# Kernel optimization log

Measured on AMD Instinct MI355X. Metric: run time of the kernel, lower is better.

Reference implementation:

```python
import jax, jax.numpy as jnp
import numpy as np

HIDDEN = 4096
NUM_HEADS = 32
HEAD_DIM = HIDDEN // NUM_HEADS
B, S = 2, 2048
ROPE_BASE = 10000.0


def setup_inputs() -> dict:
    key = jax.random.key(0)
    k1, k2, k3, k4 = jax.random.split(key, 4)
    hidden_states = jax.random.normal(k1, (B, S, HIDDEN), dtype=jnp.float32)
    positions = jnp.tile(jnp.arange(S, dtype=jnp.int32)[None, :], (B, 1))
    W_qkv = jax.random.normal(k2, (HIDDEN, 3 * HIDDEN), dtype=jnp.float32) * (HIDDEN ** -0.5)
    b_qkv = jax.random.normal(k3, (3 * HIDDEN,), dtype=jnp.float32) * 0.02
    W_o = jax.random.normal(k4, (HIDDEN, HIDDEN), dtype=jnp.float32) * (HIDDEN ** -0.5)
    return {"hidden_states": hidden_states, "positions": positions,
            "W_qkv": W_qkv, "b_qkv": b_qkv, "W_o": W_o}


def _rope(x, positions):
    # x: [B, S, H, D]; GPT-NeoX style full-dim rotary (rotary_dim = head_dim)
    half = HEAD_DIM // 2
    inv_freq = 1.0 / (ROPE_BASE ** (jnp.arange(0, half, dtype=jnp.float32) * 2.0 / HEAD_DIM))
    ang = positions.astype(jnp.float32)[:, :, None] * inv_freq[None, None, :]  # [B,S,half]
    cos = jnp.cos(ang)[:, :, None, :]  # [B,S,1,half]
    sin = jnp.sin(ang)[:, :, None, :]
    x1, x2 = x[..., :half], x[..., half:]
    return jnp.concatenate([x1 * cos - x2 * sin, x2 * cos + x1 * sin], axis=-1)


def reference(hidden_states, positions, W_qkv, b_qkv, W_o):
    qkv = jnp.einsum('bsh,hk->bsk', hidden_states, W_qkv) + b_qkv
    q, k, v = jnp.split(qkv, 3, axis=-1)
    q = q.reshape(B, S, NUM_HEADS, HEAD_DIM)
    k = k.reshape(B, S, NUM_HEADS, HEAD_DIM)
    v = v.reshape(B, S, NUM_HEADS, HEAD_DIM)
    q = _rope(q, positions)
    k = _rope(k, positions)
    scale = HEAD_DIM ** -0.5
    scores = jnp.einsum('bqhd,bkhd->bhqk', q, k) * scale  # [B,H,S,S]
    causal = jnp.tril(jnp.ones((S, S), dtype=bool))
    scores = jnp.where(causal[None, None], scores, jnp.float32(-1e30))
    probs = jax.nn.softmax(scores, axis=-1)
    ctx = jnp.einsum('bhqk,bkhd->bqhd', probs, v).reshape(B, S, HIDDEN)
    return jnp.einsum('bsh,ho->bso', ctx, W_o)
```

## Files before the change

### kernel.cpp

```cpp
#include <hip/hip_runtime.h>
#include <stdint.h>

#define HID 4096
#define NHD 32
#define HD  128
#define BB  2
#define SS  2048
#define BSZ (BB*SS)
#define N3  (3*HID)

typedef __bf16 bf16x8 __attribute__((ext_vector_type(8)));
typedef __bf16 bf16x4 __attribute__((ext_vector_type(4)));
typedef float  f32x4  __attribute__((ext_vector_type(4)));

#define MFMA16(A,B,C) __builtin_amdgcn_mfma_f32_16x16x32_bf16((A),(B),(C),0,0,0)

__device__ __forceinline__ void gl_lds16(const __bf16* g, __bf16* l) {
  __builtin_amdgcn_global_load_lds(
      (__attribute__((address_space(1))) void*)g,
      (__attribute__((address_space(3))) void*)l, 16, 0, 0);
}

__device__ __forceinline__ void block_bar() {
  __builtin_amdgcn_sched_barrier(0);
  __builtin_amdgcn_s_barrier();
  __builtin_amdgcn_sched_barrier(0);
}
#define LGKM0() do { asm volatile("s_waitcnt lgkmcnt(0)" ::: "memory"); \
                     __builtin_amdgcn_sched_barrier(0); } while (0)
#define VMC(n)  do { asm volatile("s_waitcnt vmcnt(" #n ")" ::: "memory"); \
                     __builtin_amdgcn_sched_barrier(0); } while (0)

__global__ void cvt_bf16(const float* __restrict__ in, __bf16* __restrict__ out, int n) {
  int i = (blockIdx.x * blockDim.x + threadIdx.x) * 4;
  if (i >= n) return;
  float4 v = *(const float4*)(in + i);
  bf16x4 r;
  r[0] = (__bf16)v.x; r[1] = (__bf16)v.y; r[2] = (__bf16)v.z; r[3] = (__bf16)v.w;
  *(bf16x4*)(out + i) = r;
}

__global__ void transp_cvt(const float* __restrict__ in, __bf16* __restrict__ out,
                           int R, int C) {
  __shared__ float t[64 * 65];
  int c0 = blockIdx.x * 64, r0 = blockIdx.y * 64;
  int tx = threadIdx.x & 15, ty = threadIdx.x >> 4;
  for (int j = 0; j < 4; ++j) {
    float4 v = *(const float4*)(in + (size_t)(r0 + ty + 16 * j) * C + c0 + tx * 4);
    float* d = t + (ty + 16 * j) * 65 + tx * 4;
    d[0] = v.x; d[1] = v.y; d[2] = v.z; d[3] = v.w;
  }
  __syncthreads();
  for (int j = 0; j < 4; ++j) {
    int cc = ty + 16 * j;
    bf16x4 o4;
    for (int e = 0; e < 4; ++e) o4[e] = (__bf16)t[(tx * 4 + e) * 65 + cc];
    *(bf16x4*)(out + (size_t)(c0 + cc) * R + r0 + tx * 4) = o4;
  }
}


__device__ __forceinline__ void ld_a4(bf16x8 a[4][2], const __bf16* base, int row, int quad) {
#pragma unroll
  for (int m = 0; m < 4; ++m) {
    const int rr = row + m * 16;
    const int sw = rr & 7;
#pragma unroll
    for (int kk = 0; kk < 2; ++kk)
      a[m][kk] = *(const bf16x8*)(base + rr * 64 + ((kk * 4 + quad) ^ sw) * 8);
  }
}
__device__ __forceinline__ void ld_b2(bf16x8 b[2][2], const __bf16* base, int row, int quad) {
#pragma unroll
  for (int n = 0; n < 2; ++n) {
    const int rr = row + n * 16;
    const int sw = rr & 7;
#pragma unroll
    for (int kk = 0; kk < 2; ++kk)
      b[n][kk] = *(const bf16x8*)(base + rr * 64 + ((kk * 4 + quad) ^ sw) * 8);
  }
}
__device__ __forceinline__ void mma_quad(f32x4 acc[8][4], bf16x8 a[4][2],
                                         bf16x8 b[2][2], int mh, int nh) {
  __builtin_amdgcn_s_setprio(1);
#pragma unroll
  for (int m = 0; m < 4; ++m)
#pragma unroll
    for (int n = 0; n < 2; ++n) {
      f32x4 c = acc[mh * 4 + m][nh * 2 + n];
      c = MFMA16(a[m][0], b[n][0], c);
      c = MFMA16(a[m][1], b[n][1], c);
      acc[mh * 4 + m][nh * 2 + n] = c;
    }
  __builtin_amdgcn_s_setprio(0);
}

__device__ __forceinline__ void core256(const __bf16* __restrict__ Ab,
                                        const __bf16* __restrict__ Bb,
                                        int K, __bf16* smem, f32x4 acc[8][4]) {
  const int tid  = threadIdx.x;
  const int wave = tid >> 6, lane = tid & 63;
  const int quad = lane >> 4, l15 = lane & 15;
  const int arow = ((wave >> 2) * 64) + l15;
  const int brow = ((wave & 3) * 32) + l15;
  const int NKT = K >> 6, NIT = NKT >> 1;

  __bf16* aBuf[2] = { smem,          smem + 16384 };
  __bf16* bBuf[2] = { smem + 32768,  smem + 49152 };

  const int off0 = tid * 16, off1 = off0 + 8192;
  const int r0 = off0 >> 7, r1 = off1 >> 7;
  const int sO0 = r0 * K + ((((off0 >> 4) & 7) ^ (r0 & 7)) * 8);
  const int sO1 = r1 * K + ((((off1 >> 4) & 7) ^ (r1 & 7)) * 8);
  const int d0 = off0 >> 1, d1 = off1 >> 1;

#define STG_A(buf, half, kt) do { \
    const __bf16* s_ = Ab + (size_t)(half) * 128 * K + (size_t)(kt) * 64; \
    gl_lds16(s_ + sO0, aBuf[buf] + (half) * 8192 + d0); \
    gl_lds16(s_ + sO1, aBuf[buf] + (half) * 8192 + d1); } while (0)
#define STG_B(buf, half, kt) do { \
    const __bf16* s_ = Bb + (size_t)(half) * 128 * K + (size_t)(kt) * 64; \
    gl_lds16(s_ + sO0, bBuf[buf] + (half) * 8192 + d0); \
    gl_lds16(s_ + sO1, bBuf[buf] + (half) * 8192 + d1); } while (0)

  bf16x8 a_r[4][2], bn0[2][2], bn1[2][2];

  STG_A(0, 0, 0); STG_B(0, 0, 0); STG_B(0, 1, 0); STG_A(0, 1, 0);
  STG_A(1, 0, 1); STG_B(1, 0, 1); STG_B(1, 1, 1);
  VMC(6);
  block_bar();

  for (int i = 0; i < NIT; ++i) {
    const bool last = (i == NIT - 1);
    const int t1 = 2 * i + 1, t2 = 2 * i + 2, t3 = 2 * i + 3;

    ld_a4(a_r, aBuf[0],        arow, quad);
    ld_b2(bn0, bBuf[0],        brow, quad);
    STG_A(1, 1, t1);
    block_bar(); LGKM0();
    mma_quad(acc, a_r, bn0, 0, 0);
    block_bar();

    ld_b2(bn1, bBuf[0] + 8192, brow, quad);
    if (!last) STG_A(0, 0, t2);
    block_bar(); LGKM0();
    mma_quad(acc, a_r, bn1, 0, 1);
    block_bar();

    ld_a4(a_r, aBuf[0] + 8192, arow, quad);
    if (!last) STG_B(0, 0, t2);
    block_bar(); LGKM0();
    mma_quad(acc, a_r, bn1, 1, 1);
    block_bar();

    if (!last) STG_B(0, 1, t2);
    block_bar();
    mma_quad(acc, a_r, bn0, 1, 0);
    if (last) { VMC(0); } else { VMC(6); }
    block_bar();

    ld_a4(a_r, aBuf[1],        arow, quad);
    ld_b2(bn0, bBuf[1],        brow, quad);
    if (!last) STG_A(0, 1, t2);
    block_bar(); LGKM0();
    mma_quad(acc, a_r, bn0, 0, 0);
    block_bar();

    ld_b2(bn1, bBuf[1] + 8192, brow, quad);
    if (!last) STG_A(1, 0, t3);
    block_bar(); LGKM0();
    mma_quad(acc, a_r, bn1, 0, 1);
    block_bar();

    ld_a4(a_r, aBuf[1] + 8192, arow, quad);
    if (!last) STG_B(1, 0, t3);
    block_bar(); LGKM0();
    mma_quad(acc, a_r, bn1, 1, 1);
    block_bar();

    if (!last) STG_B(1, 1, t3);
    block_bar();
    mma_quad(acc, a_r, bn0, 1, 0);
    VMC(6);
    block_bar();
  }
#undef STG_A
#undef STG_B
}

__device__ __forceinline__ int eswz(int r, int c) {
  return r * 256 + ((((c >> 3) ^ (r & 31) ^ (r >> 5)) & 31) * 8) + (c & 7);
}

__global__ __launch_bounds__(512, 2) void gemm_qkv(
    const __bf16* __restrict__ A, const __bf16* __restrict__ Bt,
    const float* __restrict__ bias, const int* __restrict__ pos,
    __bf16* __restrict__ qr, __bf16* __restrict__ kr, __bf16* __restrict__ vt,
    int M, int N, int K) {
  __shared__ __bf16 smem[65536];
  const int tid = threadIdx.x;
  const int wave = tid >> 6, lane = tid & 63;
  const int quad = lane >> 4, l15 = lane & 15;
  const int wm = (wave >> 2) * 64, wn = (wave & 3) * 32;

  const int orig = blockIdx.x;
  const int swz = (orig & 7) * 96 + (orig >> 3);
  const int m0 = (swz & 15) * 256;
  const int n0 = (swz >> 4) * 256;

  f32x4 acc[8][4];
#pragma unroll
  for (int i = 0; i < 8; ++i)
#pragma unroll
    for (int j = 0; j < 4; ++j) acc[i][j] = (f32x4){0.f, 0.f, 0.f, 0.f};

  core256(A + (size_t)m0 * K, Bt + (size_t)n0 * K, K, smem, acc);

#pragma unroll
  for (int ni = 0; ni < 4; ++ni) {
    const int scol = (ni >> 1) * 128 + wn + (ni & 1) * 16 + l15;
    const float bv = bias[n0 + scol];
#pragma unroll
    for (int mi = 0; mi < 8; ++mi) {
      const int rbase = (mi >> 2) * 128 + wm + (mi & 3) * 16 + quad * 4;
#pragma unroll
      for (int rr = 0; rr < 4; ++rr)
        smem[eswz(rbase + rr, scol)] = (__bf16)(acc[mi][ni][rr] + bv);
    }
  }
  __syncthreads();

  const int reg = n0 >> 12;
  const int h0  = (n0 & 4095) >> 7;
  const int b   = m0 >> 11;
  const int s0  = m0 & 2047;

  if (reg == 2) {
    __bf16* dst = vt + (size_t)(b * NHD + h0) * HD * SS;
    const int sg = tid & 31, cb = tid >> 5;
    for (int p = 0; p < 16; ++p) {
      const int c = cb + 16 * p;
      bf16x8 v8;
#pragma unroll
      for (int e = 0; e < 8; ++e) v8[e] = smem[eswz(sg * 8 + e, c)];
      *(bf16x8*)(dst + (size_t)(c >> 7) * HD * SS + (size_t)(c & 127) * SS +
                 s0 + sg * 8) = v8;
    }
  } else {
    __bf16* dst = (reg == 0 ? qr : kr) + (size_t)(b * NHD + h0) * SS * HD;
    const float osc = (reg == 0) ? 0.08838834764831845f : 1.0f;
    const int d2 = tid & 63, rb = (tid >> 6) * 32;
    const float freq = expf(-0.14391156831212787f * (float)d2);
    for (int i = 0; i < 32; ++i) {
      const int r = rb + i;
      const float p = (float)pos[b * SS + s0 + r];
      float sn, cs;
      sincosf(p * freq, &sn, &cs);
#pragma unroll
      for (int hs = 0; hs < 2; ++hs) {
        const float x1 = (float)smem[eswz(r, hs * 128 + d2)];
        const float x2 = (float)smem[eswz(r, hs * 128 + d2 + 64)];
        __bf16* dr = dst + (size_t)hs * SS * HD + (size_t)(s0 + r) * HD;
        dr[d2]      = (__bf16)((x1 * cs - x2 * sn) * osc);
        dr[d2 + 64] = (__bf16)((x2 * cs + x1 * sn) * osc);
      }
    }
  }
}

__global__ __launch_bounds__(512, 2) void gemm_bt(
    const __bf16* __restrict__ A, const __bf16* __restrict__ Bt,
    float* __restrict__ Cout, int M, int N, int K) {
  __shared__ __bf16 smem[65536];
  const int tid = threadIdx.x;
  const int wave = tid >> 6, lane = tid & 63;
  const int quad = lane >> 4, l15 = lane & 15;
  const int wm = (wave >> 2) * 64, wn = (wave & 3) * 32;

  const int orig = blockIdx.x;
  const int swz = (orig & 7) * 32 + (orig >> 3);
  const int m0 = (swz & 15) * 256;
  const int n0 = (swz >> 4) * 256;

  f32x4 acc[8][4];
#pragma unroll
  for (int i = 0; i < 8; ++i)
#pragma unroll
    for (int j = 0; j < 4; ++j) acc[i][j] = (f32x4){0.f, 0.f, 0.f, 0.f};

  core256(A + (size_t)m0 * K, Bt + (size_t)n0 * K, K, smem, acc);

#pragma unroll
  for (int mi = 0; mi < 8; ++mi) {
    const int row = m0 + (mi >> 2) * 128 + wm + (mi & 3) * 16 + quad * 4;
#pragma unroll
    for (int ni = 0; ni < 4; ++ni) {
      const int col = n0 + (ni >> 1) * 128 + wn + (ni & 1) * 16 + l15;
#pragma unroll
      for (int rr = 0; rr < 4; ++rr)
        Cout[(size_t)(row + rr) * N + col] = acc[mi][ni][rr];
    }
  }
}

__global__ __launch_bounds__(256, 2) void flash_attn(
    const __bf16* __restrict__ qr, const __bf16* __restrict__ kr,
    const __bf16* __restrict__ vt, __bf16* __restrict__ ctx) {
  __shared__ __bf16 sKP[4 * 32 * 136];
  __shared__ __bf16 sV[128 * 128];
  const int bh = blockIdx.x;
  const int qt = 15 - blockIdx.y;
  const int b = bh >> 5, h = bh & 31;
  const int tid = threadIdx.x;
  const int wave = tid >> 6, lane = tid & 63;
  const int quad = lane >> 4, l15 = lane & 15;
  const int q0 = qt * 128;

  const __bf16* qbase = qr + (size_t)bh * SS * HD;
  const __bf16* kbase = kr + (size_t)bh * SS * HD;
  const __bf16* vbase = vt + (size_t)bh * HD * SS;
  __bf16* sK = sKP;
  __bf16* pw = sKP + wave * (32 * 136);

  bf16x8 qf[2][4];
  for (int im = 0; im < 2; ++im) {
    int row = q0 + wave * 32 + im * 16 + l15;
    for (int ks = 0; ks < 4; ++ks)
      qf[im][ks] = *(const bf16x8*)(qbase + (size_t)row * HD + ks * 32 + quad * 8);
  }

  f32x4 o[2][8];
  for (int im = 0; im < 2; ++im)
    for (int jd = 0; jd < 8; ++jd)
      o[im][jd] = (f32x4){0.f, 0.f, 0.f, 0.f};
  float l_i[2][4];
  for (int im = 0; im < 2; ++im)
    for (int rg = 0; rg < 4; ++rg) l_i[im][rg] = 0.f;

  for (int kt = 0; kt <= qt; ++kt) {
    const int k0 = kt * 128;
    __syncthreads();
    for (int i = 0; i < 8; ++i) {
      int off = tid * 16 + i * 4096;
      int r  = off >> 8;
      int cl = (off >> 4) & 15;
      int cg = (cl & 8) | ((cl & 7) ^ (r & 7));
      gl_lds16(kbase + (size_t)(k0 + r) * HD + cg * 8, sK + (off >> 1));
      gl_lds16(vbase + (size_t)r * SS + k0 + cg * 8,   sV + (off >> 1));
    }
    __syncthreads();

    f32x4 s[2][8];
    for (int im = 0; im < 2; ++im)
      for (int jn = 0; jn < 8; ++jn)
        s[im][jn] = (f32x4){0.f, 0.f, 0.f, 0.f};
    for (int ks = 0; ks < 4; ++ks) {
      bf16x8 kf[8];
      for (int jn = 0; jn < 8; ++jn) {
        int row = jn * 16 + l15;
        int c = ks * 4 + quad;
        int p = (c & 8) | ((c & 7) ^ (row & 7));
        kf[jn] = *(const bf16x8*)(sK + row * 128 + p * 8);
      }
      for (int im = 0; im < 2; ++im)
        for (int jn = 0; jn < 8; ++jn)
          s[im][jn] = MFMA16(qf[im][ks], kf[jn], s[im][jn]);
    }
    __syncthreads();

    const bool diag = (kt == qt);
    for (int im = 0; im < 2; ++im)
      for (int rg = 0; rg < 4; ++rg) {
        int rowg = q0 + wave * 32 + im * 16 + quad * 4 + rg;
        float rs = 0.f;
        for (int jn = 0; jn < 8; ++jn) {
          float p = (diag && (k0 + jn * 16 + l15) > rowg)
                        ? 0.f : __expf(s[im][jn][rg]);
          s[im][jn][rg] = p;
          rs += p;
        }
        for (int d = 1; d < 16; d <<= 1) rs += __shfl_xor(rs, d);
        l_i[im][rg] += rs;
      }

    for (int im = 0; im < 2; ++im)
      for (int jn = 0; jn < 8; ++jn)
        for (int rg = 0; rg < 4; ++rg)
          pw[(im * 16 + quad * 4 + rg) * 136 + jn * 16 + l15] =
              (__bf16)s[im][jn][rg];

    for (int ks = 0; ks < 4; ++ks) {
      bf16x8 pf[2], vf[8];
      for (int im = 0; im < 2; ++im)
        pf[im] = *(const bf16x8*)(pw + (im * 16 + l15) * 136 + ks * 32 + quad * 8);
      for (int jd = 0; jd < 8; ++jd) {
        int row = jd * 16 + l15;
        int c = ks * 4 + quad;
        int p = (c & 8) | ((c & 7) ^ (row & 7));
        vf[jd] = *(const bf16x8*)(sV + row * 128 + p * 8);
      }
      for (int im = 0; im < 2; ++im)
        for (int jd = 0; jd < 8; ++jd)
          o[im][jd] = MFMA16(pf[im], vf[jd], o[im][jd]);
    }
  }

  __bf16* cb = ctx + (size_t)(b * SS) * HID + h * HD;
  for (int im = 0; im < 2; ++im)
    for (int rg = 0; rg < 4; ++rg) {
      float inv = 1.0f / l_i[im][rg];
      int row = q0 + wave * 32 + im * 16 + quad * 4 + rg;
      for (int jd = 0; jd < 8; ++jd)
        cb[(size_t)row * HID + jd * 16 + l15] = (__bf16)(o[im][jd][rg] * inv);
    }
}

extern "C" void kernel_launch(void* const* d_in, const int* in_sizes, int n_in,
                              void* d_out, int out_size, void* d_ws, size_t ws_size,
                              hipStream_t stream) {
  const float* hs   = (const float*)d_in[0];
  const int*   pos  = (const int*)d_in[1];
  const float* Wqkv = (const float*)d_in[2];
  const float* bqkv = (const float*)d_in[3];
  const float* Wo   = (const float*)d_in[4];

  char* ws = (char*)d_ws;
  const size_t M32 = 33554432;
  __bf16* hsb   = (__bf16*)(ws);
  __bf16* wqkvT = (__bf16*)(ws + M32);
  __bf16* woT   = (__bf16*)(ws + 4 * M32);
  __bf16* qr    = (__bf16*)(ws + 5 * M32);
  __bf16* kr    = (__bf16*)(ws + 6 * M32);
  __bf16* vt    = (__bf16*)(ws + 7 * M32);
  __bf16* ctx   = hsb;

  cvt_bf16<<<(BSZ * HID) / 1024, 256, 0, stream>>>(hs, hsb, BSZ * HID);
  transp_cvt<<<dim3(N3 / 64, HID / 64), 256, 0, stream>>>(Wqkv, wqkvT, HID, N3);
  transp_cvt<<<dim3(HID / 64, HID / 64), 256, 0, stream>>>(Wo, woT, HID, HID);
  gemm_qkv<<<768, 512, 0, stream>>>(hsb, wqkvT, bqkv, pos, qr, kr, vt,
                                    BSZ, N3, HID);
  flash_attn<<<dim3(BB * NHD, SS / 128), 256, 0, stream>>>(qr, kr, vt, ctx);
  gemm_bt<<<256, 512, 0, stream>>>(ctx, woT, (float*)d_out, BSZ, HID, HID);
}
```

Measured before the change: 964.8 us.

## Double-buffer K tiles and split attention KV loop into 64-key steps

The flash attention kernel now iterates over 64-key tiles and double-buffers K in LDS, prefetching the next K tile while computing the current one. V loads are issued early and waited on with vmcnt just before the PV product, replacing full syncthreads barriers. The P scratch buffer gets its own XOR-swizzled layout to avoid bank conflicts. In exchange there are more loop iterations and barriers per key, and correctness now depends on exact vmcnt accounting.

```diff
diff --git a/kernel.cpp b/kernel.cpp
--- a/kernel.cpp
+++ b/kernel.cpp
@@ -306,8 +306,9 @@
 __global__ __launch_bounds__(256, 2) void flash_attn(
     const __bf16* __restrict__ qr, const __bf16* __restrict__ kr,
     const __bf16* __restrict__ vt, __bf16* __restrict__ ctx) {
-  __shared__ __bf16 sKP[4 * 32 * 136];
-  __shared__ __bf16 sV[128 * 128];
+  __shared__ __bf16 sK[2][64 * 128];
+  __shared__ __bf16 sV[128 * 64];
+  __shared__ __bf16 sP[4][32 * 64];
   const int bh = blockIdx.x;
   const int qt = 15 - blockIdx.y;
   const int b = bh >> 5, h = bh & 31;
@@ -315,12 +316,31 @@
   const int wave = tid >> 6, lane = tid & 63;
   const int quad = lane >> 4, l15 = lane & 15;
   const int q0 = qt * 128;
+  const int NT = 2 * qt + 2;
 
   const __bf16* qbase = qr + (size_t)bh * SS * HD;
   const __bf16* kbase = kr + (size_t)bh * SS * HD;
   const __bf16* vbase = vt + (size_t)bh * HD * SS;
-  __bf16* sK = sKP;
-  __bf16* pw = sKP + wave * (32 * 136);
+  __bf16* pw = &sP[wave][0];
+
+#define STG_K(buf_, kt_) do {                                         \
+    const __bf16* kb_ = kbase + (size_t)(kt_) * 64 * HD;              \
+    _Pragma("unroll")                                                 \
+    for (int i_ = 0; i_ < 4; ++i_) {                                  \
+      int off_ = tid * 16 + i_ * 4096;                                \
+      int r_ = off_ >> 8, cl_ = (off_ >> 4) & 15;                     \
+      int cg_ = (cl_ & 8) | ((cl_ & 7) ^ (r_ & 7));                   \
+      gl_lds16(kb_ + (size_t)r_ * HD + cg_ * 8, &sK[buf_][0] + (off_ >> 1)); \
+    } } while (0)
+#define STG_V(kt_) do {                                               \
+    const __bf16* vb_ = vbase + (size_t)(kt_) * 64;                   \
+    _Pragma("unroll")                                                 \
+    for (int i_ = 0; i_ < 4; ++i_) {                                  \
+      int off_ = tid * 16 + i_ * 4096;                                \
+      int r_ = off_ >> 7, cl_ = (off_ >> 4) & 7;                      \
+      int cg_ = cl_ ^ (r_ & 7);                                       \
+      gl_lds16(vb_ + (size_t)r_ * SS + cg_ * 8, &sV[0] + (off_ >> 1)); \
+    } } while (0)
 
   bf16x8 qf[2][4];
   for (int im = 0; im < 2; ++im) {
@@ -337,43 +357,43 @@
   for (int im = 0; im < 2; ++im)
     for (int rg = 0; rg < 4; ++rg) l_i[im][rg] = 0.f;
 
-  for (int kt = 0; kt <= qt; ++kt) {
-    const int k0 = kt * 128;
-    __syncthreads();
-    for (int i = 0; i < 8; ++i) {
-      int off = tid * 16 + i * 4096;
-      int r  = off >> 8;
-      int cl = (off >> 4) & 15;
-      int cg = (cl & 8) | ((cl & 7) ^ (r & 7));
-      gl_lds16(kbase + (size_t)(k0 + r) * HD + cg * 8, sK + (off >> 1));
-      gl_lds16(vbase + (size_t)r * SS + k0 + cg * 8,   sV + (off >> 1));
-    }
-    __syncthreads();
-
-    f32x4 s[2][8];
+  STG_K(0, 0);
+
+  for (int kt = 0; kt < NT; ++kt) {
+    const int k0 = kt * 64;
+    const bool more = (kt + 1 < NT);
+
+    block_bar();
+    STG_V(kt);
+    if (more) STG_K((kt + 1) & 1, kt + 1);
+    if (more) { VMC(8); } else { VMC(4); }
+    block_bar();
+
+    const __bf16* sKc = &sK[kt & 1][0];
+
+    f32x4 s[2][4];
     for (int im = 0; im < 2; ++im)
-      for (int jn = 0; jn < 8; ++jn)
+      for (int jn = 0; jn < 4; ++jn)
         s[im][jn] = (f32x4){0.f, 0.f, 0.f, 0.f};
     for (int ks = 0; ks < 4; ++ks) {
-      bf16x8 kf[8];
-      for (int jn = 0; jn < 8; ++jn) {
+      bf16x8 kf[4];
+      for (int jn = 0; jn < 4; ++jn) {
         int row = jn * 16 + l15;
         int c = ks * 4 + quad;
         int p = (c & 8) | ((c & 7) ^ (row & 7));
-        kf[jn] = *(const bf16x8*)(sK + row * 128 + p * 8);
+        kf[jn] = *(const bf16x8*)(sKc + row * 128 + p * 8);
       }
       for (int im = 0; im < 2; ++im)
-        for (int jn = 0; jn < 8; ++jn)
+        for (int jn = 0; jn < 4; ++jn)
           s[im][jn] = MFMA16(qf[im][ks], kf[jn], s[im][jn]);
     }
-    __syncthreads();
-
-    const bool diag = (kt == qt);
+
+    const bool diag = (kt >= 2 * qt);
     for (int im = 0; im < 2; ++im)
       for (int rg = 0; rg < 4; ++rg) {
         int rowg = q0 + wave * 32 + im * 16 + quad * 4 + rg;
         float rs = 0.f;
-        for (int jn = 0; jn < 8; ++jn) {
+        for (int jn = 0; jn < 4; ++jn) {
           float p = (diag && (k0 + jn * 16 + l15) > rowg)
                         ? 0.f : __expf(s[im][jn][rg]);
           s[im][jn][rg] = p;
@@ -384,26 +404,36 @@
       }
 
     for (int im = 0; im < 2; ++im)
-      for (int jn = 0; jn < 8; ++jn)
-        for (int rg = 0; rg < 4; ++rg)
-          pw[(im * 16 + quad * 4 + rg) * 136 + jn * 16 + l15] =
+      for (int jn = 0; jn < 4; ++jn)
+        for (int rg = 0; rg < 4; ++rg) {
+          int row = im * 16 + quad * 4 + rg;
+          int c = jn * 2 + (l15 >> 3);
+          pw[row * 64 + ((c ^ (row & 7)) * 8) + (l15 & 7)] =
               (__bf16)s[im][jn][rg];
-
-    for (int ks = 0; ks < 4; ++ks) {
+        }
+    LGKM0();
+    if (more) { VMC(4); } else { VMC(0); }
+    block_bar();
+
+    for (int ks = 0; ks < 2; ++ks) {
       bf16x8 pf[2], vf[8];
-      for (int im = 0; im < 2; ++im)
-        pf[im] = *(const bf16x8*)(pw + (im * 16 + l15) * 136 + ks * 32 + quad * 8);
+      for (int im = 0; im < 2; ++im) {
+        int row = im * 16 + l15;
+        pf[im] = *(const bf16x8*)(pw + row * 64 +
+                                  (((ks * 4 + quad) ^ (row & 7)) * 8));
+      }
       for (int jd = 0; jd < 8; ++jd) {
         int row = jd * 16 + l15;
-        int c = ks * 4 + quad;
-        int p = (c & 8) | ((c & 7) ^ (row & 7));
-        vf[jd] = *(const bf16x8*)(sV + row * 128 + p * 8);
+        vf[jd] = *(const bf16x8*)(&sV[0] + row * 64 +
+                                  (((ks * 4 + quad) ^ (row & 7)) * 8));
       }
       for (int im = 0; im < 2; ++im)
         for (int jd = 0; jd < 8; ++jd)
           o[im][jd] = MFMA16(pf[im], vf[jd], o[im][jd]);
     }
   }
+#undef STG_K
+#undef STG_V
 
   __bf16* cb = ctx + (size_t)(b * SS) * HID + h * HD;
   for (int im = 0; im < 2; ++im)
```

After: 955.4 us. Within noise of the previous version (-1.0%).
